# Kernel optimization log

Measured on AMD Instinct MI355X. Metric: run time of the kernel, lower is better.

The kernel has to match this reference:

```python
import jax, jax.numpy as jnp
import numpy as np

N_NODES = 100000
N_EDGES = 1600000
N_GRAPHS = 64
F_IN = 128      # num_node_features
H = 64          # hidden_dim
H2 = 2 * H      # hidden_dim * 2
IMG = 50176
MLP0 = 1024
N_CLASSES = 38


def gcn_conv(x, src, dst, W, b, num_nodes):
    """PyG GCNConv: add self-loops, symmetric D^-1/2 (A+I) D^-1/2 normalization."""
    h = x @ W  # transform first: [N, out]
    loop = jnp.arange(num_nodes)
    s = jnp.concatenate([src, loop])
    d = jnp.concatenate([dst, loop])
    deg = jax.ops.segment_sum(jnp.ones_like(s, dtype=h.dtype), d, num_segments=num_nodes)
    dinv = jax.lax.rsqrt(jnp.maximum(deg, 1.0))  # deg >= 1 due to self-loops
    norm = dinv[s] * dinv[d]                     # [E+N]
    msg = h[s] * norm[:, None]                   # gather: [E+N, out]
    return jax.ops.segment_sum(msg, d, num_segments=num_nodes) + b


def setup_inputs() -> dict:
    key = jax.random.key(0)
    ks = jax.random.split(key, 16)
    s = 0.02
    x = jax.random.normal(ks[0], (N_NODES, F_IN), dtype=jnp.float32)
    edge_index = jax.random.randint(ks[1], (2, N_EDGES), 0, N_NODES)
    img_feature = jax.random.normal(ks[2], (N_GRAPHS, IMG), dtype=jnp.float32)
    batch = jnp.sort(jax.random.randint(ks[3], (N_NODES,), 0, N_GRAPHS))
    return {
        "x": x, "edge_index": edge_index, "img_feature": img_feature, "batch": batch,
        "W1": jax.random.normal(ks[4], (F_IN, H2), dtype=jnp.float32) * s,
        "b1": jnp.zeros((H2,), dtype=jnp.float32),
        "W2": jax.random.normal(ks[5], (H2, H), dtype=jnp.float32) * s,
        "b2": jnp.zeros((H,), dtype=jnp.float32),
        "Wm0": jax.random.normal(ks[6], (IMG, MLP0), dtype=jnp.float32) * s,
        "bm0": jnp.zeros((MLP0,), dtype=jnp.float32),
        "Wm1": jax.random.normal(ks[7], (MLP0, H), dtype=jnp.float32) * s,
        "bm1": jnp.zeros((H,), dtype=jnp.float32),
        "Wmx": jax.random.normal(ks[8], (H, H), dtype=jnp.float32) * s,
        "bmx": jnp.zeros((H,), dtype=jnp.float32),
        "Wfc": jax.random.normal(ks[9], (2 * H, N_CLASSES), dtype=jnp.float32) * s,
        "bfc": jnp.zeros((N_CLASSES,), dtype=jnp.float32),
    }


def reference(x, edge_index, img_feature, batch,
              W1, b1, W2, b2, Wm0, bm0, Wm1, bm1, Wmx, bmx, Wfc, bfc):
    src, dst = edge_index[0], edge_index[1]
    # image branch: 50176 -> 1024 -> hidden_dim (no activations in original code)
    x0 = (img_feature @ Wm0 + bm0) @ Wm1 + bm1          # [B, H]
    # graph branch
    h = jax.nn.relu(gcn_conv(x, src, dst, W1, b1, N_NODES))   # [N, 2H]
    h = jax.nn.relu(gcn_conv(h, src, dst, W2, b2, N_NODES))   # [N, H]
    g = jax.ops.segment_sum(h, batch, num_segments=N_GRAPHS)  # global_add_pool [B, H]
    g = g @ Wmx + bmx
    xt = jnp.concatenate([x0, g], axis=1)                # [B, 2H]
    logits = xt @ Wfc + bfc                              # [B, num_classes]
    return jax.nn.log_softmax(logits, axis=1)
```

## Files before the change

### kernel.cpp

```cpp
#include <hip/hip_runtime.h>
#include <math.h>

#define N_NODES 100000
#define N_EDGES 1600000
#define NGR 64
#define IMG_F 50176
#define NCLS 38
#define KSPLIT 49

#define NBUCK 196
#define NB_BUCK 391
#define CELLCAP 64
#define BCAP 9216
#define EPB 16

#define NB_IMG 196
#define NB_GCN1 1563
#define NB_AGG 6250
#define NB_FRONT (NB_IMG + NB_GCN1 + NB_BUCK)

typedef short bf16x8 __attribute__((ext_vector_type(8)));
typedef float f32x4 __attribute__((ext_vector_type(4)));
typedef unsigned int uint;

__device__ __forceinline__ uint pk2(float a, float b) {
  uint ua = __float_as_uint(a), ub = __float_as_uint(b);
  ua = (ua + 0x7fffu + ((ua >> 16) & 1u)) >> 16;
  ub = (ub + 0x7fffu + ((ub >> 16) & 1u)) >> 16;
  return ua | (ub << 16);
}
__device__ __forceinline__ unsigned short f2bf(float x) {
  uint u = __float_as_uint(x);
  u = (u + 0x7fffu + ((u >> 16) & 1u)) >> 16;
  return (unsigned short)u;
}
__device__ __forceinline__ float bflo(uint u) { return __uint_as_float(u << 16); }
__device__ __forceinline__ float bfhi(uint u) { return __uint_as_float(u & 0xffff0000u); }

__device__ __forceinline__ int lower_bound_i(const int* __restrict__ a, int n, int v) {
  int lo = 0, hi = n;
  while (lo < hi) { int mid = (lo + hi) >> 1; if (a[mid] < v) lo = mid + 1; else hi = mid; }
  return lo;
}

__device__ __forceinline__ void role_bucket(char* smemc, int blk,
    const int* __restrict__ src, const int* __restrict__ dst,
    uint* __restrict__ ebuf, int* __restrict__ cnt) {
  int* lhist = (int*)smemc;
  int* lcur  = lhist + 256;
  const int t = threadIdx.x;
  lhist[t] = 0; lcur[t] = 0;
  __syncthreads();
  const int e0 = blk * (EPB * 256);
  uint p[EPB]; int k[EPB];
#pragma unroll
  for (int j = 0; j < EPB; j++) {
    int e = e0 + j * 256 + t;
    if (e < N_EDGES) {
      int s = src[e], d = dst[e];
      p[j] = (uint)s | ((uint)(d & 511) << 17);
      k[j] = d >> 9;
      atomicAdd(&lhist[k[j]], 1);
    } else k[j] = -1;
  }
  __syncthreads();
#pragma unroll
  for (int j = 0; j < EPB; j++) {
    if (k[j] >= 0) {
      int pos = atomicAdd(&lcur[k[j]], 1);
      if (pos < CELLCAP)
        ebuf[((size_t)k[j] * NB_BUCK + blk) * CELLCAP + pos] = p[j];
    }
  }
  __syncthreads();
  if (t < NBUCK) {
    int c = lhist[t];
    cnt[t * NB_BUCK + blk] = (c > CELLCAP) ? CELLCAP : c;
  }
}

__device__ __forceinline__ void role_binfill(char* smemc, int b,
    const uint* __restrict__ ebuf, const int* __restrict__ cnt,
    int* __restrict__ deg, int* __restrict__ row_lo,
    float* __restrict__ dinv, int* __restrict__ csr) {
  int* scnt = (int*)smemc;
  int* soff = scnt + 512;
  int* sdeg = soff + 512;
  int* scur = sdeg + 512;
  uint* sedge = (uint*)(scur + 512);
  const int t = threadIdx.x;
  const int i0 = t, i1 = t + 256;
  int c0 = (i0 < NB_BUCK) ? cnt[b * NB_BUCK + i0] : 0;
  int c1 = (i1 < NB_BUCK) ? cnt[b * NB_BUCK + i1] : 0;
  scnt[i0] = c0; scnt[i1] = c1;
  scur[i0] = c0; scur[i1] = c1;
  __syncthreads();
  for (int off = 1; off < 512; off <<= 1) {
    int v0 = (i0 >= off) ? scnt[i0 - off] : 0;
    int v1 = (i1 >= off) ? scnt[i1 - off] : 0;
    __syncthreads();
    scnt[i0] += v0; scnt[i1] += v1;
    __syncthreads();
  }
  soff[i0] = scnt[i0] - c0;
  soff[i1] = scnt[i1] - c1;
  sdeg[i0] = 0; sdeg[i1] = 0;
  __syncthreads();
  const int grp = t >> 4, lane = t & 15;
  for (int c = grp; c < NB_BUCK; c += 16) {
    int off = soff[c], num = scur[c];
    const uint* cb = &ebuf[((size_t)b * NB_BUCK + c) * CELLCAP];
    for (int j = lane; j < num; j += 16) {
      int pos = off + j;
      if (pos < BCAP) {
        uint e = cb[j];
        sedge[pos] = e;
        atomicAdd(&sdeg[e >> 17], 1);
      }
    }
  }
  __syncthreads();
  int total = scnt[511];
  if (total > BCAP) total = BCAP;
  int d0 = sdeg[i0], d1 = sdeg[i1];
  for (int off = 1; off < 512; off <<= 1) {
    int v0 = (i0 >= off) ? sdeg[i0 - off] : 0;
    int v1 = (i1 >= off) ? sdeg[i1 - off] : 0;
    __syncthreads();
    sdeg[i0] += v0; sdeg[i1] += v1;
    __syncthreads();
  }
  int ex0 = sdeg[i0] - d0, ex1 = sdeg[i1] - d1;
  int n0 = b * 512 + i0, n1 = b * 512 + i1;
  if (n0 < N_NODES) { deg[n0] = d0; row_lo[n0] = b * BCAP + ex0; dinv[n0] = rsqrtf((float)d0 + 1.0f); }
  if (n1 < N_NODES) { deg[n1] = d1; row_lo[n1] = b * BCAP + ex1; dinv[n1] = rsqrtf((float)d1 + 1.0f); }
  scur[i0] = ex0; scur[i1] = ex1;
  __syncthreads();
  for (int j = t; j < total; j += 256) {
    uint e = sedge[j];
    int pos = atomicAdd(&scur[e >> 17], 1);
    csr[(size_t)b * BCAP + pos] = (int)(e & 0x1FFFFu);
  }
}

__device__ __forceinline__ void role_img(char* smemc, int b,
    const float* __restrict__ A, const float* __restrict__ B,
    float* __restrict__ partial) {
  short* Bl = (short*)smemc;
  const int tid = threadIdx.x;
  const int l = tid & 63, w = tid >> 6;
  const int col0 = (b & 3) * 256;
  const int kbase = (b >> 2) * 1024;
  const int kq_l = l >> 4, rr_l = l & 15;
  f32x4 acc[16];
#pragma unroll
  for (int ct = 0; ct < 16; ct++) acc[ct] = (f32x4)(0.f);

  for (int st = 0; st < 16; st++) {
    int k0 = kbase + st * 64;
    bf16x8 af[2];
#pragma unroll
    for (int kst = 0; kst < 2; kst++) {
      const float* ap = &A[(size_t)(w * 16 + rr_l) * IMG_F + k0 + (kst * 4 + kq_l) * 8];
      float4 f0 = *(const float4*)ap;
      float4 f1 = *(const float4*)(ap + 4);
      uint au[4] = {pk2(f0.x, f0.y), pk2(f0.z, f0.w), pk2(f1.x, f1.y), pk2(f1.z, f1.w)};
      af[kst] = *(bf16x8*)au;
    }
    __syncthreads();
    {
      int col4 = tid & 63, koB = tid >> 6;
#pragma unroll
      for (int itb = 0; itb < 2; itb++) {
        int ko = koB + itb * 4;
        const float* bp = &B[(size_t)(k0 + ko * 8) * 1024 + col0 + col4 * 4];
        float fb[8][4];
#pragma unroll
        for (int i2 = 0; i2 < 8; i2++)
          *(float4*)&fb[i2][0] = *(const float4*)(bp + (size_t)i2 * 1024);
        int kst = ko >> 2, kq = ko & 3;
#pragma unroll
        for (int c2 = 0; c2 < 4; c2++) {
          int col = col4 * 4 + c2;
          int ct = col >> 4, colin = col & 15;
          int ci = ((kst * 4 + kq) * 16 + (ct ^ kq)) * 16 + colin;
          uint4 u = make_uint4(pk2(fb[0][c2], fb[1][c2]), pk2(fb[2][c2], fb[3][c2]),
                               pk2(fb[4][c2], fb[5][c2]), pk2(fb[6][c2], fb[7][c2]));
          *(uint4*)&Bl[ci * 8] = u;
        }
      }
    }
    __syncthreads();
#pragma unroll
    for (int kst = 0; kst < 2; kst++) {
#pragma unroll
      for (int ct = 0; ct < 16; ct++) {
        bf16x8 bf = *(bf16x8*)&Bl[(((kst * 4 + kq_l) * 16 + (ct ^ kq_l)) * 16 + rr_l) * 8];
        acc[ct] = __builtin_amdgcn_mfma_f32_16x16x32_bf16(af[kst], bf, acc[ct], 0, 0, 0);
      }
    }
  }
  float* P = partial + (size_t)(b >> 2) * 65536;
#pragma unroll
  for (int ct = 0; ct < 16; ct++)
#pragma unroll
    for (int rg = 0; rg < 4; rg++) {
      int row = w * 16 + (l >> 4) * 4 + rg;
      int col = col0 + ct * 16 + (l & 15);
      P[row * 1024 + col] = acc[ct][rg];
    }
}

template<int N, bool RELU_BIAS, bool BF16_IN, bool SCALE>
__device__ __forceinline__ void role_gcn(char* smemc, int row0,
    const void* __restrict__ Ain, const float* __restrict__ W,
    const float* __restrict__ abias, const float* __restrict__ dinv,
    unsigned short* __restrict__ C, int M) {
  constexpr int NT16 = N / 16;
  short* Wl = (short*)smemc;
  const int tid = threadIdx.x;
  const int l = tid & 63, w = tid >> 6;
  const int kq_l = l >> 4, rr_l = l & 15;

#pragma unroll
  for (int it = 0; it < (N == 128 ? 2 : 1); it++) {
    int mt = tid + it * 256;
    int col4 = mt % (N / 4), ko = mt / (N / 4);
    float fb[8][4];
#pragma unroll
    for (int i2 = 0; i2 < 8; i2++)
      *(float4*)&fb[i2][0] = *(const float4*)&W[(size_t)(ko * 8 + i2) * N + col4 * 4];
    int kst = ko >> 2, kq = ko & 3;
#pragma unroll
    for (int c2 = 0; c2 < 4; c2++) {
      int col = col4 * 4 + c2;
      int ct = col >> 4, colin = col & 15;
      int ci = ((kst * 4 + kq) * NT16 + (ct ^ kq)) * 16 + colin;
      uint4 u = make_uint4(pk2(fb[0][c2], fb[1][c2]), pk2(fb[2][c2], fb[3][c2]),
                           pk2(fb[4][c2], fb[5][c2]), pk2(fb[6][c2], fb[7][c2]));
      *(uint4*)&Wl[ci * 8] = u;
    }
  }

  const int row = row0 + w * 16 + rr_l;
  const bool valid = row < M;
  bf16x8 af[4];
#pragma unroll
  for (int kst = 0; kst < 4; kst++) {
    int ko = kst * 4 + kq_l;
    float f[8] = {0.f, 0.f, 0.f, 0.f, 0.f, 0.f, 0.f, 0.f};
    if (valid) {
      if constexpr (BF16_IN) {
        uint4 u = *(const uint4*)((const uint*)Ain + (size_t)row * 64 + ko * 4);
        f[0] = bflo(u.x); f[1] = bfhi(u.x); f[2] = bflo(u.y); f[3] = bfhi(u.y);
        f[4] = bflo(u.z); f[5] = bfhi(u.z); f[6] = bflo(u.w); f[7] = bfhi(u.w);
      } else {
        const float* ap = (const float*)Ain + (size_t)row * 128 + ko * 8;
        *(float4*)&f[0] = *(const float4*)ap;
        *(float4*)&f[4] = *(const float4*)(ap + 4);
      }
      if (RELU_BIAS) {
        const float* bp = &abias[ko * 8];
        float bb[8];
        *(float4*)&bb[0] = *(const float4*)bp;
        *(float4*)&bb[4] = *(const float4*)(bp + 4);
#pragma unroll
        for (int j = 0; j < 8; j++) f[j] = fmaxf(f[j] + bb[j], 0.f);
      }
    }
    uint au[4] = {pk2(f[0], f[1]), pk2(f[2], f[3]), pk2(f[4], f[5]), pk2(f[6], f[7])};
    af[kst] = *(bf16x8*)au;
  }
  __syncthreads();

  f32x4 acc[NT16];
#pragma unroll
  for (int ct = 0; ct < NT16; ct++) acc[ct] = (f32x4)(0.f);
#pragma unroll
  for (int kst = 0; kst < 4; kst++) {
#pragma unroll
    for (int ct = 0; ct < NT16; ct++) {
      bf16x8 bf = *(bf16x8*)&Wl[(((kst * 4 + kq_l) * NT16 + (ct ^ kq_l)) * 16 + rr_l) * 8];
      acc[ct] = __builtin_amdgcn_mfma_f32_16x16x32_bf16(af[kst], bf, acc[ct], 0, 0, 0);
    }
  }
#pragma unroll
  for (int rg = 0; rg < 4; rg++) {
    int orow = row0 + w * 16 + (l >> 4) * 4 + rg;
    if (orow < M) {
      float dsc = SCALE ? dinv[orow] : 1.f;
#pragma unroll
      for (int ct = 0; ct < NT16; ct++)
        C[(size_t)orow * N + ct * 16 + (l & 15)] = f2bf(acc[ct][rg] * dsc);
    }
  }
}

template<int F, int VEC, bool SRCS>
__device__ __forceinline__ void role_agg(int nb,
    const unsigned short* __restrict__ h, const float* __restrict__ dinv,
    const int* __restrict__ row_lo, const int* __restrict__ deg,
    const int* __restrict__ csr_src, unsigned short* __restrict__ out) {
  constexpr int L = F / VEC;
  constexpr int NPB = 256 / L;
  constexpr int NU = VEC / 2;
  int n = nb * NPB + threadIdx.x / L;
  int lane = threadIdx.x % L;
  if (n >= N_NODES) return;
  const uint* hu = (const uint*)h;
  const int rs = F / 2;
  float dn = dinv[n];
  float acc[VEC];
  uint r0[NU];
  if constexpr (VEC == 8) *(uint4*)r0 = *(const uint4*)&hu[(size_t)n * rs + lane * NU];
  else                    *(uint2*)r0 = *(const uint2*)&hu[(size_t)n * rs + lane * NU];
#pragma unroll
  for (int j = 0; j < NU; j++) {
    float sw = SRCS ? dn : 1.f;
    acc[2*j] = sw * bflo(r0[j]); acc[2*j+1] = sw * bfhi(r0[j]);
  }
  int lo = row_lo[n], hi = lo + deg[n];
  int i = lo;
  for (; i + 8 <= hi; i += 8) {
    int ss[8];
#pragma unroll
    for (int u = 0; u < 8; u++) ss[u] = csr_src[i + u];
    uint a[8][NU];
#pragma unroll
    for (int u = 0; u < 8; u++) {
      if constexpr (VEC == 8) *(uint4*)a[u] = *(const uint4*)&hu[(size_t)ss[u] * rs + lane * NU];
      else                    *(uint2*)a[u] = *(const uint2*)&hu[(size_t)ss[u] * rs + lane * NU];
    }
    if constexpr (SRCS) {
      float wv[8];
#pragma unroll
      for (int u = 0; u < 8; u++) wv[u] = dinv[ss[u]];
#pragma unroll
      for (int u = 0; u < 8; u++)
#pragma unroll
        for (int j = 0; j < NU; j++) {
          acc[2*j]   = fmaf(wv[u], bflo(a[u][j]), acc[2*j]);
          acc[2*j+1] = fmaf(wv[u], bfhi(a[u][j]), acc[2*j+1]);
        }
    } else {
#pragma unroll
      for (int u = 0; u < 8; u++)
#pragma unroll
        for (int j = 0; j < NU; j++) {
          acc[2*j]   += bflo(a[u][j]);
          acc[2*j+1] += bfhi(a[u][j]);
        }
    }
  }
  for (; i + 2 <= hi; i += 2) {
    int s0 = csr_src[i], s1 = csr_src[i + 1];
    uint a0[NU], a1[NU];
    if constexpr (VEC == 8) {
      *(uint4*)a0 = *(const uint4*)&hu[(size_t)s0 * rs + lane * NU];
      *(uint4*)a1 = *(const uint4*)&hu[(size_t)s1 * rs + lane * NU];
    } else {
      *(uint2*)a0 = *(const uint2*)&hu[(size_t)s0 * rs + lane * NU];
      *(uint2*)a1 = *(const uint2*)&hu[(size_t)s1 * rs + lane * NU];
    }
    float w0 = SRCS ? dinv[s0] : 1.f, w1 = SRCS ? dinv[s1] : 1.f;
#pragma unroll
    for (int j = 0; j < NU; j++) {
      acc[2*j]   = fmaf(w0, bflo(a0[j]), fmaf(w1, bflo(a1[j]), acc[2*j]));
      acc[2*j+1] = fmaf(w0, bfhi(a0[j]), fmaf(w1, bfhi(a1[j]), acc[2*j+1]));
    }
  }
  if (i < hi) {
    int s0 = csr_src[i];
    uint a0[NU];
    if constexpr (VEC == 8) *(uint4*)a0 = *(const uint4*)&hu[(size_t)s0 * rs + lane * NU];
    else                    *(uint2*)a0 = *(const uint2*)&hu[(size_t)s0 * rs + lane * NU];
    float w0 = SRCS ? dinv[s0] : 1.f;
#pragma unroll
    for (int j = 0; j < NU; j++) {
      acc[2*j]   = fmaf(w0, bflo(a0[j]), acc[2*j]);
      acc[2*j+1] = fmaf(w0, bfhi(a0[j]), acc[2*j+1]);
    }
  }
  uint o[NU];
#pragma unroll
  for (int j = 0; j < NU; j++) o[j] = pk2(dn * acc[2*j], dn * acc[2*j+1]);
  uint* op = (uint*)out + (size_t)n * rs + lane * NU;
  if constexpr (VEC == 8) *(uint4*)op = *(uint4*)o;
  else                    *(uint2*)op = *(uint2*)o;
}

__global__ __launch_bounds__(256)
void k_front(const float* __restrict__ img, const float* __restrict__ Wm0,
             float* __restrict__ partial,
             const float* __restrict__ x, const float* __restrict__ W1,
             unsigned short* __restrict__ bufA,
             const int* __restrict__ src, const int* __restrict__ dst,
             uint* __restrict__ ebuf, int* __restrict__ cnt) {
  __shared__ __align__(16) char smem[32768];
  int vb = (int)(((long long)blockIdx.x * 997) % NB_FRONT);
  if (vb < NB_IMG) {
    role_img(smem, vb, img, Wm0, partial);
  } else if (vb < NB_IMG + NB_GCN1) {
    role_gcn<128, false, false, false>(smem, (vb - NB_IMG) * 64, x, W1, nullptr,
                                       nullptr, bufA, N_NODES);
  } else {
    role_bucket(smem, vb - NB_IMG - NB_GCN1, src, dst, ebuf, cnt);
  }
}

__global__ __launch_bounds__(256)
void k_mid(const uint* __restrict__ ebuf, const int* __restrict__ cnt,
           int* __restrict__ deg, int* __restrict__ row_lo,
           float* __restrict__ dinv, int* __restrict__ csr,
           const float* __restrict__ partial, const float* __restrict__ bm0,
           float* __restrict__ tmp1) {
  __shared__ __align__(16) char smem[45056];
  int b = blockIdx.x;
  if (b < NBUCK) {
    role_binfill(smem, b, ebuf, cnt, deg, row_lo, dinv, csr);
  } else {
    int i = (b - NBUCK) * 256 + threadIdx.x;
    float s = bm0[i & 1023];
    for (int ks = 0; ks < KSPLIT; ks++) s += partial[(size_t)ks * 65536 + i];
    tmp1[i] = s;
  }
}

__global__ __launch_bounds__(256)
void k_aggA(const unsigned short* __restrict__ h, const float* __restrict__ dinv,
            const int* __restrict__ row_lo, const int* __restrict__ deg,
            const int* __restrict__ csr, unsigned short* __restrict__ outp,
            const float* __restrict__ T, const float* __restrict__ Wm1,
            const float* __restrict__ bm1, float* __restrict__ x0) {
  __shared__ float red[4][64];
  int b = blockIdx.x;
  if (b < 64) {
    int r = b;
    int c = threadIdx.x & 63;
    int q = threadIdx.x >> 6;
    float acc = 0.f;
#pragma unroll 8
    for (int k = q; k < 1024; k += 4)
      acc = fmaf(T[r * 1024 + k], Wm1[k * 64 + c], acc);
    red[q][c] = acc;
    __syncthreads();
    if (q == 0) x0[r * 64 + c] = red[0][c] + red[1][c] + red[2][c] + red[3][c] + bm1[c];
  } else {
    role_agg<128, 8, true>(b - 64, h, dinv, row_lo, deg, csr, outp);
  }
}

__global__ __launch_bounds__(256)
void k_gcn2(const unsigned short* __restrict__ Ain, const float* __restrict__ W,
            const float* __restrict__ abias, const float* __restrict__ dinv,
            unsigned short* __restrict__ C) {
  __shared__ __align__(16) char smem[16384];
  role_gcn<64, true, true, true>(smem, blockIdx.x * 64, Ain, W, abias, dinv, C, N_NODES);
}

__global__ __launch_bounds__(256)
void k_agg2(const unsigned short* __restrict__ h, const float* __restrict__ dinv,
            const int* __restrict__ row_lo, const int* __restrict__ deg,
            const int* __restrict__ csr, unsigned short* __restrict__ outp) {
  role_agg<64, 4, false>(blockIdx.x, h, dinv, row_lo, deg, csr, outp);
}

__global__ __launch_bounds__(256)
void k_tail(const unsigned short* __restrict__ h2, const float* __restrict__ b2,
            const int* __restrict__ batch, const float* __restrict__ x0,
            const float* __restrict__ Wmx, const float* __restrict__ bmx,
            const float* __restrict__ Wfc, const float* __restrict__ bfc,
            float* __restrict__ out) {
  int b = blockIdx.x;
  int f = threadIdx.x & 63;
  int q = threadIdx.x >> 6;
  __shared__ float red[4][64];
  __shared__ float sx[128];
  __shared__ float slog[NCLS];
  __shared__ float sred;
  int lo = lower_bound_i(batch, N_NODES, b);
  int hi = lower_bound_i(batch, N_NODES, b + 1);
  float bias = b2[f];
  float acc = 0.f;
  for (int i = lo + q; i < hi; i += 4)
    acc += fmaxf(__uint_as_float((uint)h2[(size_t)i * 64 + f] << 16) + bias, 0.f);
  red[q][f] = acc;
  __syncthreads();
  if (q == 0) red[0][f] = red[0][f] + red[1][f] + red[2][f] + red[3][f];
  __syncthreads();
  int c = threadIdx.x;
  if (c < 64) {
    float a2 = bmx[c];
#pragma unroll 8
    for (int k = 0; k < 64; k++) a2 = fmaf(red[0][k], Wmx[k * 64 + c], a2);
    sx[64 + c] = a2;
    sx[c] = x0[b * 64 + c];
  }
  __syncthreads();
  float lg = 0.f;
  if (c < NCLS) {
    lg = bfc[c];
#pragma unroll 8
    for (int k = 0; k < 128; k++) lg = fmaf(sx[k], Wfc[k * NCLS + c], lg);
    slog[c] = lg;
  }
  __syncthreads();
  if (c == 0) {
    float m = -1e30f;
    for (int j = 0; j < NCLS; j++) m = fmaxf(m, slog[j]);
    float s = 0.f;
    for (int j = 0; j < NCLS; j++) s += expf(slog[j] - m);
    sred = m + logf(s);
  }
  __syncthreads();
  if (c < NCLS) out[b * NCLS + c] = lg - sred;
}

extern "C" void kernel_launch(void* const* d_in, const int* in_sizes, int n_in,
                              void* d_out, int out_size, void* d_ws, size_t ws_size,
                              hipStream_t stream) {
  const float* x    = (const float*)d_in[0];
  const int*   edge = (const int*)d_in[1];
  const float* img  = (const float*)d_in[2];
  const int*   batch= (const int*)d_in[3];
  const float* W1   = (const float*)d_in[4];
  const float* b1   = (const float*)d_in[5];
  const float* W2   = (const float*)d_in[6];
  const float* b2   = (const float*)d_in[7];
  const float* Wm0  = (const float*)d_in[8];
  const float* bm0  = (const float*)d_in[9];
  const float* Wm1  = (const float*)d_in[10];
  const float* bm1  = (const float*)d_in[11];
  const float* Wmx  = (const float*)d_in[12];
  const float* bmx  = (const float*)d_in[13];
  const float* Wfc  = (const float*)d_in[14];
  const float* bfc  = (const float*)d_in[15];
  float* out = (float*)d_out;
  const int* srcp = edge;
  const int* dstp = edge + N_EDGES;

  char* ws = (char*)d_ws;
  size_t off = 0;
  auto alloc = [&](size_t bytes) {
    void* p = ws + off;
    off += (bytes + 255) & ~(size_t)255;
    return p;
  };
  int*   cnt    = (int*)  alloc((size_t)NBUCK * NB_BUCK * 4);
  uint*  ebuf   = (uint*) alloc((size_t)NBUCK * NB_BUCK * CELLCAP * 4);
  int*   csr    = (int*)  alloc((size_t)NBUCK * BCAP * 4);
  int*   deg    = (int*)  alloc((size_t)N_NODES * 4);
  int*   row_lo = (int*)  alloc((size_t)N_NODES * 4);
  float* dinv   = (float*)alloc((size_t)N_NODES * 4);
  unsigned short* bufA = (unsigned short*)alloc((size_t)N_NODES * 128 * 2);
  unsigned short* bufB = (unsigned short*)alloc((size_t)N_NODES * 128 * 2);
  float* tmp1   = (float*)alloc(64 * 1024 * 4);
  float* x0     = (float*)alloc(64 * 64 * 4);
  float* partial = (float*)bufB;
  (void)ws_size; (void)in_sizes; (void)n_in; (void)out_size;

  k_front<<<NB_FRONT, 256, 0, stream>>>(
      img, Wm0, partial, x, W1, bufA, srcp, dstp, ebuf, cnt);
  k_mid<<<NBUCK + 256, 256, 0, stream>>>(
      ebuf, cnt, deg, row_lo, dinv, csr, partial, bm0, tmp1);
  k_aggA<<<64 + NB_AGG, 256, 0, stream>>>(
      bufA, dinv, row_lo, deg, csr, bufB, tmp1, Wm1, bm1, x0);
  k_gcn2<<<NB_GCN1, 256, 0, stream>>>(bufB, W2, b1, dinv, bufA);
  k_agg2<<<NB_AGG, 256, 0, stream>>>(bufA, dinv, row_lo, deg, csr, bufB);
  k_tail<<<NGR, 256, 0, stream>>>(bufB, b2, batch, x0, Wmx, bmx, Wfc, bfc, out);
}
```

Measured before the change: 649.7 us.

## Fuse layer-1 aggregation with GCN2 transform and pooling into aggregation

Layer-1 neighbor aggregation is fused with bias+ReLU and the W2 matmul in one kernel, so the intermediate aggregated features are kept in LDS instead of written out and re-read. Layer-2 aggregation is fused with bias+ReLU and global add-pool using per-block segmented reduction and atomics into a zeroed accumulator, which removes the tail's binary search and node scan. The A operands of the image and GCN1 MFMA tiles are now staged through swizzled LDS with coalesced loads, and the front kernel's block-index scrambling is removed. This adds larger LDS footprints and float atomics, which make the pooled sums order-dependent.

Measured after the change: 528.4 us. 18.7% less time.

```diff
diff --git a/kernel.cpp b/kernel.cpp
--- a/kernel.cpp
+++ b/kernel.cpp
@@ -16,7 +16,7 @@
 
 #define NB_IMG 196
 #define NB_GCN1 1563
-#define NB_AGG 6250
+#define NB_AGGP 6250
 #define NB_FRONT (NB_IMG + NB_GCN1 + NB_BUCK)
 
 typedef short bf16x8 __attribute__((ext_vector_type(8)));
@@ -36,12 +36,6 @@
 }
 __device__ __forceinline__ float bflo(uint u) { return __uint_as_float(u << 16); }
 __device__ __forceinline__ float bfhi(uint u) { return __uint_as_float(u & 0xffff0000u); }
-
-__device__ __forceinline__ int lower_bound_i(const int* __restrict__ a, int n, int v) {
-  int lo = 0, hi = n;
-  while (lo < hi) { int mid = (lo + hi) >> 1; if (a[mid] < v) lo = mid + 1; else hi = mid; }
-  return lo;
-}
 
 __device__ __forceinline__ void role_bucket(char* smemc, int blk,
     const int* __restrict__ src, const int* __restrict__ dst,
@@ -146,7 +140,8 @@
 __device__ __forceinline__ void role_img(char* smemc, int b,
     const float* __restrict__ A, const float* __restrict__ B,
     float* __restrict__ partial) {
-  short* Bl = (short*)smemc;
+  short* Al = (short*)smemc;
+  short* Bl = (short*)(smemc + 8192);
   const int tid = threadIdx.x;
   const int l = tid & 63, w = tid >> 6;
   const int col0 = (b & 3) * 256;
@@ -158,16 +153,20 @@
 
   for (int st = 0; st < 16; st++) {
     int k0 = kbase + st * 64;
-    bf16x8 af[2];
-#pragma unroll
-    for (int kst = 0; kst < 2; kst++) {
-      const float* ap = &A[(size_t)(w * 16 + rr_l) * IMG_F + k0 + (kst * 4 + kq_l) * 8];
+    __syncthreads();
+#pragma unroll
+    for (int it = 0; it < 2; it++) {
+      int c = tid + it * 256;
+      int r = c >> 3, ko = c & 7;
+      const float* ap = &A[(size_t)r * IMG_F + k0 + ko * 8];
       float4 f0 = *(const float4*)ap;
       float4 f1 = *(const float4*)(ap + 4);
-      uint au[4] = {pk2(f0.x, f0.y), pk2(f0.z, f0.w), pk2(f1.x, f1.y), pk2(f1.z, f1.w)};
-      af[kst] = *(bf16x8*)au;
-    }
-    __syncthreads();
+      int kst = ko >> 2, kq = ko & 3, rt = r >> 4, rr = r & 15;
+      int ci = ((kst * 4 + kq) * 4 + (rt ^ kq)) * 16 + rr;
+      uint4 u = make_uint4(pk2(f0.x, f0.y), pk2(f0.z, f0.w),
+                           pk2(f1.x, f1.y), pk2(f1.z, f1.w));
+      *(uint4*)&Al[ci * 8] = u;
+    }
     {
       int col4 = tid & 63, koB = tid >> 6;
 #pragma unroll
@@ -193,10 +192,11 @@
     __syncthreads();
 #pragma unroll
     for (int kst = 0; kst < 2; kst++) {
+      bf16x8 af = *(bf16x8*)&Al[(((kst * 4 + kq_l) * 4 + (w ^ kq_l)) * 16 + rr_l) * 8];
 #pragma unroll
       for (int ct = 0; ct < 16; ct++) {
         bf16x8 bf = *(bf16x8*)&Bl[(((kst * 4 + kq_l) * 16 + (ct ^ kq_l)) * 16 + rr_l) * 8];
-        acc[ct] = __builtin_amdgcn_mfma_f32_16x16x32_bf16(af[kst], bf, acc[ct], 0, 0, 0);
+        acc[ct] = __builtin_amdgcn_mfma_f32_16x16x32_bf16(af, bf, acc[ct], 0, 0, 0);
       }
     }
   }
@@ -211,25 +211,41 @@
     }
 }
 
-template<int N, bool RELU_BIAS, bool BF16_IN, bool SCALE>
-__device__ __forceinline__ void role_gcn(char* smemc, int row0,
-    const void* __restrict__ Ain, const float* __restrict__ W,
-    const float* __restrict__ abias, const float* __restrict__ dinv,
-    unsigned short* __restrict__ C, int M) {
-  constexpr int NT16 = N / 16;
-  short* Wl = (short*)smemc;
+__device__ __forceinline__ void role_gcn1(char* smemc, int row0,
+    const float* __restrict__ Ain, const float* __restrict__ W,
+    unsigned short* __restrict__ C) {
+  constexpr int NT16 = 8;
+  short* Al = (short*)smemc;
+  short* Wl = (short*)(smemc + 16384);
   const int tid = threadIdx.x;
   const int l = tid & 63, w = tid >> 6;
   const int kq_l = l >> 4, rr_l = l & 15;
 
 #pragma unroll
-  for (int it = 0; it < (N == 128 ? 2 : 1); it++) {
+  for (int it = 0; it < 4; it++) {
+    int c = tid + it * 256;
+    int r = c >> 4, ko = c & 15;
+    int row = row0 + r;
+    float f[8] = {0.f, 0.f, 0.f, 0.f, 0.f, 0.f, 0.f, 0.f};
+    if (row < N_NODES) {
+      const float* ap = Ain + (size_t)row * 128 + ko * 8;
+      *(float4*)&f[0] = *(const float4*)ap;
+      *(float4*)&f[4] = *(const float4*)(ap + 4);
+    }
+    int kst = ko >> 2, kq = ko & 3, rt = r >> 4, rr = r & 15;
+    int ci = ((kst * 4 + kq) * 4 + (rt ^ kq)) * 16 + rr;
+    uint4 u = make_uint4(pk2(f[0], f[1]), pk2(f[2], f[3]),
+                         pk2(f[4], f[5]), pk2(f[6], f[7]));
+    *(uint4*)&Al[ci * 8] = u;
+  }
+#pragma unroll
+  for (int it = 0; it < 2; it++) {
     int mt = tid + it * 256;
-    int col4 = mt % (N / 4), ko = mt / (N / 4);
+    int col4 = mt % 32, ko = mt / 32;
     float fb[8][4];
 #pragma unroll
     for (int i2 = 0; i2 < 8; i2++)
-      *(float4*)&fb[i2][0] = *(const float4*)&W[(size_t)(ko * 8 + i2) * N + col4 * 4];
+      *(float4*)&fb[i2][0] = *(const float4*)&W[(size_t)(ko * 8 + i2) * 128 + col4 * 4];
     int kst = ko >> 2, kq = ko & 3;
 #pragma unroll
     for (int c2 = 0; c2 < 4; c2++) {
@@ -241,152 +257,139 @@
       *(uint4*)&Wl[ci * 8] = u;
     }
   }
-
-  const int row = row0 + w * 16 + rr_l;
-  const bool valid = row < M;
-  bf16x8 af[4];
+  __syncthreads();
+
+  f32x4 acc[NT16];
+#pragma unroll
+  for (int ct = 0; ct < NT16; ct++) acc[ct] = (f32x4)(0.f);
 #pragma unroll
   for (int kst = 0; kst < 4; kst++) {
-    int ko = kst * 4 + kq_l;
-    float f[8] = {0.f, 0.f, 0.f, 0.f, 0.f, 0.f, 0.f, 0.f};
-    if (valid) {
-      if constexpr (BF16_IN) {
-        uint4 u = *(const uint4*)((const uint*)Ain + (size_t)row * 64 + ko * 4);
-        f[0] = bflo(u.x); f[1] = bfhi(u.x); f[2] = bflo(u.y); f[3] = bfhi(u.y);
-        f[4] = bflo(u.z); f[5] = bfhi(u.z); f[6] = bflo(u.w); f[7] = bfhi(u.w);
-      } else {
-        const float* ap = (const float*)Ain + (size_t)row * 128 + ko * 8;
-        *(float4*)&f[0] = *(const float4*)ap;
-        *(float4*)&f[4] = *(const float4*)(ap + 4);
-      }
-      if (RELU_BIAS) {
-        const float* bp = &abias[ko * 8];
-        float bb[8];
-        *(float4*)&bb[0] = *(const float4*)bp;
-        *(float4*)&bb[4] = *(const float4*)(bp + 4);
-#pragma unroll
-        for (int j = 0; j < 8; j++) f[j] = fmaxf(f[j] + bb[j], 0.f);
-      }
-    }
-    uint au[4] = {pk2(f[0], f[1]), pk2(f[2], f[3]), pk2(f[4], f[5]), pk2(f[6], f[7])};
-    af[kst] = *(bf16x8*)au;
-  }
-  __syncthreads();
-
-  f32x4 acc[NT16];
-#pragma unroll
-  for (int ct = 0; ct < NT16; ct++) acc[ct] = (f32x4)(0.f);
-#pragma unroll
-  for (int kst = 0; kst < 4; kst++) {
+    bf16x8 af = *(bf16x8*)&Al[(((kst * 4 + kq_l) * 4 + (w ^ kq_l)) * 16 + rr_l) * 8];
 #pragma unroll
     for (int ct = 0; ct < NT16; ct++) {
       bf16x8 bf = *(bf16x8*)&Wl[(((kst * 4 + kq_l) * NT16 + (ct ^ kq_l)) * 16 + rr_l) * 8];
-      acc[ct] = __builtin_amdgcn_mfma_f32_16x16x32_bf16(af[kst], bf, acc[ct], 0, 0, 0);
+      acc[ct] = __builtin_amdgcn_mfma_f32_16x16x32_bf16(af, bf, acc[ct], 0, 0, 0);
+    }
+  }
+#pragma unroll
+  for (int rg = 0; rg < 4; rg++) {
+    int row = row0 + w * 16 + (l >> 4) * 4 + rg;
+    if (row < N_NODES) {
+#pragma unroll
+      for (int ct = 0; ct < NT16; ct++)
+        C[(size_t)row * 128 + ct * 16 + (l & 15)] = f2bf(acc[ct][rg]);
+    }
+  }
+}
+
+__device__ __forceinline__ void role_agg_gcn(char* smemc, int row0,
+    const unsigned short* __restrict__ h1, const float* __restrict__ dinv,
+    const int* __restrict__ row_lo, const int* __restrict__ deg,
+    const int* __restrict__ csr_src, const float* __restrict__ b1,
+    const float* __restrict__ W2, unsigned short* __restrict__ out) {
+  short* Al = (short*)smemc;
+  short* Wl = (short*)(smemc + 16384);
+  const int tid = threadIdx.x;
+  {
+    int col4 = tid & 15, ko = tid >> 4;
+    float fb[8][4];
+#pragma unroll
+    for (int i2 = 0; i2 < 8; i2++)
+      *(float4*)&fb[i2][0] = *(const float4*)&W2[(size_t)(ko * 8 + i2) * 64 + col4 * 4];
+    int kst = ko >> 2, kq = ko & 3;
+#pragma unroll
+    for (int c2 = 0; c2 < 4; c2++) {
+      int col = col4 * 4 + c2;
+      int ct = col >> 4, colin = col & 15;
+      int ci = ((kst * 4 + kq) * 4 + (ct ^ kq)) * 16 + colin;
+      uint4 u = make_uint4(pk2(fb[0][c2], fb[1][c2]), pk2(fb[2][c2], fb[3][c2]),
+                           pk2(fb[4][c2], fb[5][c2]), pk2(fb[6][c2], fb[7][c2]));
+      *(uint4*)&Wl[ci * 8] = u;
+    }
+  }
+  const int grp = tid >> 4, lane = tid & 15;
+  const uint* hu = (const uint*)h1;
+  float bb[8];
+  *(float4*)&bb[0] = *(const float4*)&b1[lane * 8];
+  *(float4*)&bb[4] = *(const float4*)&b1[lane * 8 + 4];
+#pragma unroll 1
+  for (int rnd = 0; rnd < 4; rnd++) {
+    int r = rnd * 16 + grp;
+    int n = row0 + r;
+    float f[8] = {0.f, 0.f, 0.f, 0.f, 0.f, 0.f, 0.f, 0.f};
+    if (n < N_NODES) {
+      float dn = dinv[n];
+      float acc[8];
+      uint r0[4];
+      *(uint4*)r0 = *(const uint4*)&hu[(size_t)n * 64 + lane * 4];
+#pragma unroll
+      for (int j = 0; j < 4; j++) { acc[2*j] = dn * bflo(r0[j]); acc[2*j+1] = dn * bfhi(r0[j]); }
+      int lo = row_lo[n], hiEnd = lo + deg[n];
+      int i = lo;
+      for (; i + 8 <= hiEnd; i += 8) {
+        int ss[8];
+#pragma unroll
+        for (int u = 0; u < 8; u++) ss[u] = csr_src[i + u];
+        uint a[8][4];
+#pragma unroll
+        for (int u = 0; u < 8; u++)
+          *(uint4*)a[u] = *(const uint4*)&hu[(size_t)ss[u] * 64 + lane * 4];
+        float wv[8];
+#pragma unroll
+        for (int u = 0; u < 8; u++) wv[u] = dinv[ss[u]];
+#pragma unroll
+        for (int u = 0; u < 8; u++)
+#pragma unroll
+          for (int j = 0; j < 4; j++) {
+            acc[2*j]   = fmaf(wv[u], bflo(a[u][j]), acc[2*j]);
+            acc[2*j+1] = fmaf(wv[u], bfhi(a[u][j]), acc[2*j+1]);
+          }
+      }
+      for (; i < hiEnd; i++) {
+        int s0 = csr_src[i];
+        uint a0[4];
+        *(uint4*)a0 = *(const uint4*)&hu[(size_t)s0 * 64 + lane * 4];
+        float w0 = dinv[s0];
+#pragma unroll
+        for (int j = 0; j < 4; j++) {
+          acc[2*j]   = fmaf(w0, bflo(a0[j]), acc[2*j]);
+          acc[2*j+1] = fmaf(w0, bfhi(a0[j]), acc[2*j+1]);
+        }
+      }
+#pragma unroll
+      for (int j = 0; j < 8; j++) f[j] = fmaxf(fmaf(dn, acc[j], bb[j]), 0.f);
+    }
+    int kst = lane >> 2, kq = lane & 3;
+    int ci = ((kst * 4 + kq) * 4 + (rnd ^ kq)) * 16 + grp;
+    uint4 u = make_uint4(pk2(f[0], f[1]), pk2(f[2], f[3]),
+                         pk2(f[4], f[5]), pk2(f[6], f[7]));
+    *(uint4*)&Al[ci * 8] = u;
+  }
+  __syncthreads();
+  const int l = tid & 63, w = tid >> 6;
+  const int kq_l = l >> 4, rr_l = l & 15;
+  f32x4 acc2[4];
+#pragma unroll
+  for (int ct = 0; ct < 4; ct++) acc2[ct] = (f32x4)(0.f);
+#pragma unroll
+  for (int kst = 0; kst < 4; kst++) {
+    bf16x8 af = *(bf16x8*)&Al[(((kst * 4 + kq_l) * 4 + (w ^ kq_l)) * 16 + rr_l) * 8];
+#pragma unroll
+    for (int ct = 0; ct < 4; ct++) {
+      bf16x8 bf = *(bf16x8*)&Wl[(((kst * 4 + kq_l) * 4 + (ct ^ kq_l)) * 16 + rr_l) * 8];
+      acc2[ct] = __builtin_amdgcn_mfma_f32_16x16x32_bf16(af, bf, acc2[ct], 0, 0, 0);
     }
   }
 #pragma unroll
   for (int rg = 0; rg < 4; rg++) {
     int orow = row0 + w * 16 + (l >> 4) * 4 + rg;
-    if (orow < M) {
-      float dsc = SCALE ? dinv[orow] : 1.f;
-#pragma unroll
-      for (int ct = 0; ct < NT16; ct++)
-        C[(size_t)orow * N + ct * 16 + (l & 15)] = f2bf(acc[ct][rg] * dsc);
-    }
-  }
-}
-
-template<int F, int VEC, bool SRCS>
-__device__ __forceinline__ void role_agg(int nb,
-    const unsigned short* __restrict__ h, const float* __restrict__ dinv,
-    const int* __restrict__ row_lo, const int* __restrict__ deg,
-    const int* __restrict__ csr_src, unsigned short* __restrict__ out) {
-  constexpr int L = F / VEC;
-  constexpr int NPB = 256 / L;
-  constexpr int NU = VEC / 2;
-  int n = nb * NPB + threadIdx.x / L;
-  int lane = threadIdx.x % L;
-  if (n >= N_NODES) return;
-  const uint* hu = (const uint*)h;
-  const int rs = F / 2;
-  float dn = dinv[n];
-  float acc[VEC];
-  uint r0[NU];
-  if constexpr (VEC == 8) *(uint4*)r0 = *(const uint4*)&hu[(size_t)n * rs + lane * NU];
-  else                    *(uint2*)r0 = *(const uint2*)&hu[(size_t)n * rs + lane * NU];
-#pragma unroll
-  for (int j = 0; j < NU; j++) {
-    float sw = SRCS ? dn : 1.f;
-    acc[2*j] = sw * bflo(r0[j]); acc[2*j+1] = sw * bfhi(r0[j]);
-  }
-  int lo = row_lo[n], hi = lo + deg[n];
-  int i = lo;
-  for (; i + 8 <= hi; i += 8) {
-    int ss[8];
-#pragma unroll
-    for (int u = 0; u < 8; u++) ss[u] = csr_src[i + u];
-    uint a[8][NU];
-#pragma unroll
-    for (int u = 0; u < 8; u++) {
-      if constexpr (VEC == 8) *(uint4*)a[u] = *(const uint4*)&hu[(size_t)ss[u] * rs + lane * NU];
-      else                    *(uint2*)a[u] = *(const uint2*)&hu[(size_t)ss[u] * rs + lane * NU];
-    }
-    if constexpr (SRCS) {
-      float wv[8];
-#pragma unroll
-      for (int u = 0; u < 8; u++) wv[u] = dinv[ss[u]];
-#pragma unroll
-      for (int u = 0; u < 8; u++)
-#pragma unroll
-        for (int j = 0; j < NU; j++) {
-          acc[2*j]   = fmaf(wv[u], bflo(a[u][j]), acc[2*j]);
-          acc[2*j+1] = fmaf(wv[u], bfhi(a[u][j]), acc[2*j+1]);
-        }
-    } else {
-#pragma unroll
-      for (int u = 0; u < 8; u++)
-#pragma unroll
-        for (int j = 0; j < NU; j++) {
-          acc[2*j]   += bflo(a[u][j]);
-          acc[2*j+1] += bfhi(a[u][j]);
-        }
-    }
-  }
-  for (; i + 2 <= hi; i += 2) {
-    int s0 = csr_src[i], s1 = csr_src[i + 1];
-    uint a0[NU], a1[NU];
-    if constexpr (VEC == 8) {
-      *(uint4*)a0 = *(const uint4*)&hu[(size_t)s0 * rs + lane * NU];
-      *(uint4*)a1 = *(const uint4*)&hu[(size_t)s1 * rs + lane * NU];
-    } else {
-      *(uint2*)a0 = *(const uint2*)&hu[(size_t)s0 * rs + lane * NU];
-      *(uint2*)a1 = *(const uint2*)&hu[(size_t)s1 * rs + lane * NU];
-    }
-    float w0 = SRCS ? dinv[s0] : 1.f, w1 = SRCS ? dinv[s1] : 1.f;
-#pragma unroll
-    for (int j = 0; j < NU; j++) {
-      acc[2*j]   = fmaf(w0, bflo(a0[j]), fmaf(w1, bflo(a1[j]), acc[2*j]));
-      acc[2*j+1] = fmaf(w0, bfhi(a0[j]), fmaf(w1, bfhi(a1[j]), acc[2*j+1]));
-    }
-  }
-  if (i < hi) {
-    int s0 = csr_src[i];
-    uint a0[NU];
-    if constexpr (VEC == 8) *(uint4*)a0 = *(const uint4*)&hu[(size_t)s0 * rs + lane * NU];
-    else                    *(uint2*)a0 = *(const uint2*)&hu[(size_t)s0 * rs + lane * NU];
-    float w0 = SRCS ? dinv[s0] : 1.f;
-#pragma unroll
-    for (int j = 0; j < NU; j++) {
-      acc[2*j]   = fmaf(w0, bflo(a0[j]), acc[2*j]);
-      acc[2*j+1] = fmaf(w0, bfhi(a0[j]), acc[2*j+1]);
-    }
-  }
-  uint o[NU];
-#pragma unroll
-  for (int j = 0; j < NU; j++) o[j] = pk2(dn * acc[2*j], dn * acc[2*j+1]);
-  uint* op = (uint*)out + (size_t)n * rs + lane * NU;
-  if constexpr (VEC == 8) *(uint4*)op = *(uint4*)o;
-  else                    *(uint2*)op = *(uint2*)o;
+    if (orow < N_NODES) {
+      float dsc = dinv[orow];
+#pragma unroll
+      for (int ct = 0; ct < 4; ct++)
+        out[(size_t)orow * 64 + ct * 16 + (l & 15)] = f2bf(acc2[ct][rg] * dsc);
+    }
+  }
 }
 
 __global__ __launch_bounds__(256)
@@ -396,15 +399,14 @@
              unsigned short* __restrict__ bufA,
              const int* __restrict__ src, const int* __restrict__ dst,
              uint* __restrict__ ebuf, int* __restrict__ cnt) {
-  __shared__ __align__(16) char smem[32768];
-  int vb = (int)(((long long)blockIdx.x * 997) % NB_FRONT);
-  if (vb < NB_IMG) {
-    role_img(smem, vb, img, Wm0, partial);
-  } else if (vb < NB_IMG + NB_GCN1) {
-    role_gcn<128, false, false, false>(smem, (vb - NB_IMG) * 64, x, W1, nullptr,
-                                       nullptr, bufA, N_NODES);
+  __shared__ __align__(16) char smem[49152];
+  int b = blockIdx.x;
+  if (b < NB_IMG) {
+    role_img(smem, b, img, Wm0, partial);
+  } else if (b < NB_IMG + NB_GCN1) {
+    role_gcn1(smem, (b - NB_IMG) * 64, x, W1, bufA);
   } else {
-    role_bucket(smem, vb - NB_IMG - NB_GCN1, src, dst, ebuf, cnt);
+    role_bucket(smem, b - NB_IMG - NB_GCN1, src, dst, ebuf, cnt);
   }
 }
 
@@ -413,25 +415,29 @@
            int* __restrict__ deg, int* __restrict__ row_lo,
            float* __restrict__ dinv, int* __restrict__ csr,
            const float* __restrict__ partial, const float* __restrict__ bm0,
-           float* __restrict__ tmp1) {
+           float* __restrict__ tmp1, float* __restrict__ gacc) {
   __shared__ __align__(16) char smem[45056];
   int b = blockIdx.x;
   if (b < NBUCK) {
     role_binfill(smem, b, ebuf, cnt, deg, row_lo, dinv, csr);
-  } else {
+  } else if (b < NBUCK + 256) {
     int i = (b - NBUCK) * 256 + threadIdx.x;
     float s = bm0[i & 1023];
     for (int ks = 0; ks < KSPLIT; ks++) s += partial[(size_t)ks * 65536 + i];
     tmp1[i] = s;
+  } else {
+    for (int j = threadIdx.x; j < NGR * 64; j += 256) gacc[j] = 0.f;
   }
 }
 
 __global__ __launch_bounds__(256)
-void k_aggA(const unsigned short* __restrict__ h, const float* __restrict__ dinv,
-            const int* __restrict__ row_lo, const int* __restrict__ deg,
-            const int* __restrict__ csr, unsigned short* __restrict__ outp,
-            const float* __restrict__ T, const float* __restrict__ Wm1,
-            const float* __restrict__ bm1, float* __restrict__ x0) {
+void k_fuse3(const unsigned short* __restrict__ h1, const float* __restrict__ dinv,
+             const int* __restrict__ row_lo, const int* __restrict__ deg,
+             const int* __restrict__ csr, const float* __restrict__ b1,
+             const float* __restrict__ W2, unsigned short* __restrict__ h2,
+             const float* __restrict__ T, const float* __restrict__ Wm1,
+             const float* __restrict__ bm1, float* __restrict__ x0) {
+  __shared__ __align__(16) char smem[32768];
   __shared__ float red[4][64];
   int b = blockIdx.x;
   if (b < 64) {
@@ -446,56 +452,84 @@
     __syncthreads();
     if (q == 0) x0[r * 64 + c] = red[0][c] + red[1][c] + red[2][c] + red[3][c] + bm1[c];
   } else {
-    role_agg<128, 8, true>(b - 64, h, dinv, row_lo, deg, csr, outp);
+    role_agg_gcn(smem, (b - 64) * 64, h1, dinv, row_lo, deg, csr, b1, W2, h2);
   }
 }
 
 __global__ __launch_bounds__(256)
-void k_gcn2(const unsigned short* __restrict__ Ain, const float* __restrict__ W,
-            const float* __restrict__ abias, const float* __restrict__ dinv,
-            unsigned short* __restrict__ C) {
-  __shared__ __align__(16) char smem[16384];
-  role_gcn<64, true, true, true>(smem, blockIdx.x * 64, Ain, W, abias, dinv, C, N_NODES);
-}
-
-__global__ __launch_bounds__(256)
-void k_agg2(const unsigned short* __restrict__ h, const float* __restrict__ dinv,
-            const int* __restrict__ row_lo, const int* __restrict__ deg,
-            const int* __restrict__ csr, unsigned short* __restrict__ outp) {
-  role_agg<64, 4, false>(blockIdx.x, h, dinv, row_lo, deg, csr, outp);
-}
-
-__global__ __launch_bounds__(256)
-void k_tail(const unsigned short* __restrict__ h2, const float* __restrict__ b2,
-            const int* __restrict__ batch, const float* __restrict__ x0,
+void k_aggpool(const unsigned short* __restrict__ h2, const float* __restrict__ dinv,
+               const int* __restrict__ row_lo, const int* __restrict__ deg,
+               const int* __restrict__ csr_src, const float* __restrict__ b2,
+               const int* __restrict__ batch, float* __restrict__ gacc) {
+  __shared__ float sacc[16][64];
+  __shared__ int sgid[16];
+  const int tid = threadIdx.x;
+  const int grp = tid >> 4, lane = tid & 15;
+  int n = blockIdx.x * 16 + grp;
+  const uint* hu = (const uint*)h2;
+  float dn = dinv[n];
+  float acc[4];
+  uint r0[2];
+  *(uint2*)r0 = *(const uint2*)&hu[(size_t)n * 32 + lane * 2];
+  acc[0] = bflo(r0[0]); acc[1] = bfhi(r0[0]); acc[2] = bflo(r0[1]); acc[3] = bfhi(r0[1]);
+  int lo = row_lo[n], hiEnd = lo + deg[n];
+  int i = lo;
+  for (; i + 8 <= hiEnd; i += 8) {
+    int ss[8];
+#pragma unroll
+    for (int u = 0; u < 8; u++) ss[u] = csr_src[i + u];
+    uint a[8][2];
+#pragma unroll
+    for (int u = 0; u < 8; u++)
+      *(uint2*)a[u] = *(const uint2*)&hu[(size_t)ss[u] * 32 + lane * 2];
+#pragma unroll
+    for (int u = 0; u < 8; u++) {
+      acc[0] += bflo(a[u][0]); acc[1] += bfhi(a[u][0]);
+      acc[2] += bflo(a[u][1]); acc[3] += bfhi(a[u][1]);
+    }
+  }
+  for (; i < hiEnd; i++) {
+    uint a0[2];
+    *(uint2*)a0 = *(const uint2*)&hu[(size_t)csr_src[i] * 32 + lane * 2];
+    acc[0] += bflo(a0[0]); acc[1] += bfhi(a0[0]);
+    acc[2] += bflo(a0[1]); acc[3] += bfhi(a0[1]);
+  }
+  float bb[4];
+  *(float4*)bb = *(const float4*)&b2[lane * 4];
+#pragma unroll
+  for (int j = 0; j < 4; j++) acc[j] = fmaxf(fmaf(dn, acc[j], bb[j]), 0.f);
+  *(float4*)&sacc[grp][lane * 4] = *(float4*)acc;
+  if (lane == 0) sgid[grp] = batch[n];
+  __syncthreads();
+  if (tid < 64) {
+    int f = tid;
+    int cur = sgid[0];
+    float s = 0.f;
+#pragma unroll
+    for (int g2 = 0; g2 < 16; g2++) {
+      int gg = sgid[g2];
+      if (gg != cur) { atomicAdd(&gacc[cur * 64 + f], s); cur = gg; s = 0.f; }
+      s += sacc[g2][f];
+    }
+    atomicAdd(&gacc[cur * 64 + f], s);
+  }
+}
+
+__global__ __launch_bounds__(64)
+void k_head(const float* __restrict__ gacc, const float* __restrict__ x0,
             const float* __restrict__ Wmx, const float* __restrict__ bmx,
             const float* __restrict__ Wfc, const float* __restrict__ bfc,
             float* __restrict__ out) {
-  int b = blockIdx.x;
-  int f = threadIdx.x & 63;
-  int q = threadIdx.x >> 6;
-  __shared__ float red[4][64];
+  int r = blockIdx.x;
+  int c = threadIdx.x;
   __shared__ float sx[128];
   __shared__ float slog[NCLS];
   __shared__ float sred;
-  int lo = lower_bound_i(batch, N_NODES, b);
-  int hi = lower_bound_i(batch, N_NODES, b + 1);
-  float bias = b2[f];
-  float acc = 0.f;
-  for (int i = lo + q; i < hi; i += 4)
-    acc += fmaxf(__uint_as_float((uint)h2[(size_t)i * 64 + f] << 16) + bias, 0.f);
-  red[q][f] = acc;
-  __syncthreads();
-  if (q == 0) red[0][f] = red[0][f] + red[1][f] + red[2][f] + red[3][f];
-  __syncthreads();
-  int c = threadIdx.x;
-  if (c < 64) {
-    float a2 = bmx[c];
+  float a2 = bmx[c];
 #pragma unroll 8
-    for (int k = 0; k < 64; k++) a2 = fmaf(red[0][k], Wmx[k * 64 + c], a2);
-    sx[64 + c] = a2;
-    sx[c] = x0[b * 64 + c];
-  }
+  for (int k = 0; k < 64; k++) a2 = fmaf(gacc[r * 64 + k], Wmx[k * 64 + c], a2);
+  sx[64 + c] = a2;
+  sx[c] = x0[r * 64 + c];
   __syncthreads();
   float lg = 0.f;
   if (c < NCLS) {
@@ -513,7 +547,7 @@
     sred = m + logf(s);
   }
   __syncthreads();
-  if (c < NCLS) out[b * NCLS + c] = lg - sred;
+  if (c < NCLS) out[r * NCLS + c] = lg - sred;
 }
 
 extern "C" void kernel_launch(void* const* d_in, const int* in_sizes, int n_in,
@@ -556,16 +590,17 @@
   unsigned short* bufB = (unsigned short*)alloc((size_t)N_NODES * 128 * 2);
   float* tmp1   = (float*)alloc(64 * 1024 * 4);
   float* x0     = (float*)alloc(64 * 64 * 4);
+  float* gacc   = (float*)alloc((size_t)NGR * 64 * 4);
   float* partial = (float*)bufB;
   (void)ws_size; (void)in_sizes; (void)n_in; (void)out_size;
 
   k_front<<<NB_FRONT, 256, 0, stream>>>(
       img, Wm0, partial, x, W1, bufA, srcp, dstp, ebuf, cnt);
-  k_mid<<<NBUCK + 256, 256, 0, stream>>>(
-      ebuf, cnt, deg, row_lo, dinv, csr, partial, bm0, tmp1);
-  k_aggA<<<64 + NB_AGG, 256, 0, stream>>>(
-      bufA, dinv, row_lo, deg, csr, bufB, tmp1, Wm1, bm1, x0);
-  k_gcn2<<<NB_GCN1, 256, 0, stream>>>(bufB, W2, b1, dinv, bufA);
-  k_agg2<<<NB_AGG, 256, 0, stream>>>(bufA, dinv, row_lo, deg, csr, bufB);
-  k_tail<<<NGR, 256, 0, stream>>>(bufB, b2, batch, x0, Wmx, bmx, Wfc, bfc, out);
-}
+  k_mid<<<NBUCK + 256 + 1, 256, 0, stream>>>(
+      ebuf, cnt, deg, row_lo, dinv, csr, partial, bm0, tmp1, gacc);
+  k_fuse3<<<64 + NB_GCN1, 256, 0, stream>>>(
+      bufA, dinv, row_lo, deg, csr, b1, W2, bufB, tmp1, Wm1, bm1, x0);
+  k_aggpool<<<NB_AGGP, 256, 0, stream>>>(
+      bufB, dinv, row_lo, deg, csr, b2, batch, gacc);
+  k_head<<<NGR, 64, 0, stream>>>(gacc, x0, Wmx, bmx, Wfc, bfc, out);
+}
```
